# Performance work log

Hardware: AMD Instinct MI355X
Metric: run time of the kernel (lower is better)

## Reference

```python
import jax, jax.numpy as jnp
import numpy as np

NTOKENS = 50257
NHID = 1024
NPC = int(np.ceil(np.sqrt(NTOKENS)))            # 225 tokens per class
NCLASSES = int(np.ceil(NTOKENS / NPC))          # 224 classes
BATCH = 1024
INITRANGE = 0.1


def setup_inputs() -> dict:
    key = jax.random.key(0)
    k1, k2, k3, k4 = jax.random.split(key, 4)
    inputs = jax.random.normal(k1, (BATCH, NHID), dtype=jnp.float32)
    labels = jax.random.randint(k2, (BATCH,), 0, NTOKENS, dtype=jnp.int64)
    layer_top_W = jax.random.uniform(k3, (NHID, NCLASSES), minval=-INITRANGE, maxval=INITRANGE, dtype=jnp.float32)
    layer_top_b = jnp.zeros((NCLASSES,), dtype=jnp.float32)
    layer_bottom_W = jax.random.uniform(k4, (NCLASSES, NHID, NPC), minval=-INITRANGE, maxval=INITRANGE, dtype=jnp.float32)
    layer_bottom_b = jnp.zeros((NCLASSES, NPC), dtype=jnp.float32)
    return {
        "inputs": inputs,
        "labels": labels,
        "layer_top_W": layer_top_W,
        "layer_top_b": layer_top_b,
        "layer_bottom_W": layer_bottom_W,
        "layer_bottom_b": layer_bottom_b,
    }


def reference(inputs, labels, layer_top_W, layer_top_b, layer_bottom_W, layer_bottom_b):
    batch_size = inputs.shape[0]
    # decompose label into (class, within-class) position; old-torch `/` on Long == floor div
    pos_top = labels // NPC            # [B]
    pos_bottom = labels % NPC          # [B]

    # top-level class distribution: [B, nclasses]
    top_logits = inputs @ layer_top_W + layer_top_b
    top_probs = jax.nn.softmax(top_logits, axis=1)

    # gather per-sample class weight slices and do batched matvec:
    # layer_bottom_W[pos_top]: [B, nhid, npc]
    bottom_logits = jnp.einsum("bd,bdc->bc", inputs, layer_bottom_W[pos_top]) + layer_bottom_b[pos_top]
    bottom_probs = jax.nn.softmax(bottom_logits, axis=1)

    rows = jnp.arange(batch_size)
    target_probs = top_probs[rows, pos_top] * bottom_probs[rows, pos_bottom]  # [B]
    return target_probs
```

## Files before the change

kernel.cpp:

```cpp
#include <hip/hip_runtime.h>
#include <math.h>

#define NTOK 50257
#define NHID 1024
#define NPC  225
#define NCLS 224
#define BATCH 1024

#define WS_ORDER_OFS 16
#define WS_ITEMS_OFS 8192
#define WS_PTOP_OFS  16384
#define MAX_ITEMS    352

__device__ __forceinline__ void group_samples(const int* __restrict__ labels,
                                              int* __restrict__ ws, int tid)
{
    __shared__ int cnt[256];
    __shared__ int scan[256];
    __shared__ int iscan[256];
    __shared__ int cur[256];

    if (tid < 256) cnt[tid] = 0;
    __syncthreads();
    for (int i = tid; i < BATCH; i += 512)
        atomicAdd(&cnt[labels[i] / NPC], 1);
    __syncthreads();

    int myc = 0, myi = 0;
    if (tid < 256) {
        myc = (tid < NCLS) ? cnt[tid] : 0;
        myi = (myc + 7) >> 3;
        scan[tid]  = myc;
        iscan[tid] = myi;
    }
    __syncthreads();
    for (int off = 1; off < 256; off <<= 1) {
        int a = 0, b = 0;
        if (tid < 256 && tid >= off) { a = scan[tid - off]; b = iscan[tid - off]; }
        __syncthreads();
        if (tid < 256) { scan[tid] += a; iscan[tid] += b; }
        __syncthreads();
    }
    if (tid < 256) {
        const int sbase = scan[tid]  - myc;
        const int ibase = iscan[tid] - myi;
        if (tid == 255) ws[0] = iscan[255];
        cur[tid] = sbase;
        int4* items = (int4*)((char*)ws + WS_ITEMS_OFS);
        if (tid < NCLS)
            for (int t = 0; t < myi; ++t)
                items[ibase + t] = make_int4(tid, sbase + 8 * t, min(8, myc - 8 * t), 0);
    }
    __syncthreads();
    int* order = ws + WS_ORDER_OFS;
    for (int i = tid; i < BATCH; i += 512) {
        int c = labels[i] / NPC;
        int p = atomicAdd(&cur[c], 1);
        order[p] = i;
    }
}

template <int LD, int COLS, bool NT>
__device__ __forceinline__ void block_matvec8_softmax(
    float* __restrict__ sm,
    const float* __restrict__ W,
    const float* __restrict__ bias,
    int wave, int lane, int nt,
    const int* __restrict__ s_ids,
    const int* __restrict__ labels,
    bool bottom,
    const float* __restrict__ ptop,
    float* __restrict__ outp)
{
    float acc[8][4];
#pragma unroll
    for (int j = 0; j < 8; ++j)
#pragma unroll
        for (int k = 0; k < 4; ++k) acc[j][k] = 0.f;

    const int c0 = lane, c1 = lane + 64, c2 = lane + 128, c3 = lane + 192;
    const bool m3 = (c3 < COLS);
    const int d0 = wave * 128;
    const float* Wr = W + (size_t)d0 * LD;

    auto ldrow = [&](int r, float* o) {
        const float* p = Wr + (size_t)r * LD;
        if (NT) {
            o[0] = __builtin_nontemporal_load(p + c0);
            o[1] = __builtin_nontemporal_load(p + c1);
            o[2] = __builtin_nontemporal_load(p + c2);
            o[3] = m3 ? __builtin_nontemporal_load(p + c3) : 0.f;
        } else {
            o[0] = p[c0]; o[1] = p[c1]; o[2] = p[c2];
            o[3] = m3 ? p[c3] : 0.f;
        }
    };

    float wbuf[4][4];
    ldrow(0, wbuf[0]); ldrow(1, wbuf[1]); ldrow(2, wbuf[2]); ldrow(3, wbuf[3]);

#pragma unroll 4
    for (int dd = 0; dd < 128; ++dd) {
        const int slot = dd & 3;
        const float cw0 = wbuf[slot][0], cw1 = wbuf[slot][1],
                    cw2 = wbuf[slot][2], cw3 = wbuf[slot][3];
        ldrow(min(dd + 4, 127), wbuf[slot]);
        const float4 a = *(const float4*)&sm[(d0 + dd) * 12 + 0];
        const float4 b = *(const float4*)&sm[(d0 + dd) * 12 + 4];
        const float xi[8] = {a.x, a.y, a.z, a.w, b.x, b.y, b.z, b.w};
#pragma unroll
        for (int j = 0; j < 8; ++j) {
            acc[j][0] = fmaf(xi[j], cw0, acc[j][0]);
            acc[j][1] = fmaf(xi[j], cw1, acc[j][1]);
            acc[j][2] = fmaf(xi[j], cw2, acc[j][2]);
            acc[j][3] = fmaf(xi[j], cw3, acc[j][3]);
        }
    }
    __syncthreads();

    float* red = sm;
    if (wave >= 4) {
#pragma unroll
        for (int j = 0; j < 8; ++j)
#pragma unroll
            for (int k = 0; k < 4; ++k) {
                int c = lane + 64 * k;
                if (c < COLS) red[((wave - 4) * 8 + j) * 232 + c] = acc[j][k];
            }
    }
    __syncthreads();
    if (wave < 4) {
#pragma unroll
        for (int j = 0; j < 8; ++j)
#pragma unroll
            for (int k = 0; k < 4; ++k) {
                int c = lane + 64 * k;
                if (c < COLS) red[(wave * 8 + j) * 232 + c] += acc[j][k];
            }
    }
    __syncthreads();

    const int j = wave;
    if (j < nt) {
        const int s = s_ids[j];
        float v[4];
#pragma unroll
        for (int k = 0; k < 4; ++k) {
            int c = lane + 64 * k;
            v[k] = (c < COLS)
                     ? (red[(0 * 8 + j) * 232 + c] + red[(1 * 8 + j) * 232 + c] +
                        red[(2 * 8 + j) * 232 + c] + red[(3 * 8 + j) * 232 + c] +
                        bias[c])
                     : -INFINITY;
        }
        float m = fmaxf(fmaxf(v[0], v[1]), fmaxf(v[2], v[3]));
        for (int o = 32; o > 0; o >>= 1) m = fmaxf(m, __shfl_xor(m, o));
        float e = expf(v[0] - m) + expf(v[1] - m) + expf(v[2] - m) + expf(v[3] - m);
        for (int o = 32; o > 0; o >>= 1) e += __shfl_xor(e, o);
        const int lab = labels[s];
        const int tgt = bottom ? (lab % NPC) : (lab / NPC);
        if (lane == (tgt & 63)) {
            float p = expf(v[tgt >> 6] - m) / e;
            outp[s] = bottom ? (ptop[s] * p) : p;
        }
    }
}

__global__ __launch_bounds__(512) void k1_top(const float* __restrict__ X,
                                              const int* __restrict__ labels,
                                              const float* __restrict__ Wt,
                                              const float* __restrict__ bt,
                                              float* __restrict__ ptop,
                                              int* __restrict__ ws)
{
    __shared__ __align__(16) float smem[12288];
    const int tid = threadIdx.x;

    if (blockIdx.x == BATCH / 8) {
        group_samples(labels, ws, tid);
        return;
    }

    const int wave = tid >> 6;
    const int lane = tid & 63;
    const int sbase = blockIdx.x * 8;

    for (int idx = tid; idx < 2048; idx += 512) {
        const int j  = idx >> 8;
        const int d4 = idx & 255;
        const float4 v = ((const float4*)&X[(size_t)(sbase + j) * NHID])[d4];
        smem[(4 * d4 + 0) * 12 + j] = v.x;
        smem[(4 * d4 + 1) * 12 + j] = v.y;
        smem[(4 * d4 + 2) * 12 + j] = v.z;
        smem[(4 * d4 + 3) * 12 + j] = v.w;
    }
    __syncthreads();

    int s_ids[8];
#pragma unroll
    for (int j = 0; j < 8; ++j) s_ids[j] = sbase + j;

    block_matvec8_softmax<NCLS, NCLS, false>(smem, Wt, bt, wave, lane, 8, s_ids,
                                             labels, false, nullptr, ptop);
}

__global__ __launch_bounds__(512) void k2_bottom(const float* __restrict__ X,
                                                 const int* __restrict__ labels,
                                                 const float* __restrict__ Wb,
                                                 const float* __restrict__ bb,
                                                 const int* __restrict__ ws,
                                                 const float* __restrict__ ptop,
                                                 float* __restrict__ out)
{
    __shared__ __align__(16) float smem[12288];
    const int nitems = ws[0];
    if ((int)blockIdx.x >= nitems) return;
    const int4 item = ((const int4*)((const char*)ws + WS_ITEMS_OFS))[blockIdx.x];
    const int cls = item.x, s0 = item.y, nt = item.z;
    const int* order = ws + WS_ORDER_OFS;

    const int tid  = threadIdx.x;
    const int wave = tid >> 6;
    const int lane = tid & 63;

    int s_ids[8];
#pragma unroll
    for (int j = 0; j < 8; ++j) s_ids[j] = (j < nt) ? order[s0 + j] : 0;

    for (int idx = tid; idx < 2048; idx += 512) {
        const int j  = idx >> 8;
        const int d4 = idx & 255;
        float4 v = make_float4(0.f, 0.f, 0.f, 0.f);
        if (j < nt) v = ((const float4*)&X[(size_t)s_ids[j] * NHID])[d4];
        smem[(4 * d4 + 0) * 12 + j] = v.x;
        smem[(4 * d4 + 1) * 12 + j] = v.y;
        smem[(4 * d4 + 2) * 12 + j] = v.z;
        smem[(4 * d4 + 3) * 12 + j] = v.w;
    }
    __syncthreads();

    const float* W = Wb + (size_t)cls * (NHID * NPC);
    block_matvec8_softmax<NPC, NPC, true>(smem, W, bb + cls * NPC, wave, lane,
                                          nt, s_ids, labels, true, ptop, out);
}

extern "C" void kernel_launch(void* const* d_in, const int* in_sizes, int n_in,
                              void* d_out, int out_size, void* d_ws, size_t ws_size,
                              hipStream_t stream)
{
    const float* X      = (const float*)d_in[0];
    const int*   labels = (const int*)  d_in[1];
    const float* Wt     = (const float*)d_in[2];
    const float* bt     = (const float*)d_in[3];
    const float* Wb     = (const float*)d_in[4];
    const float* bb     = (const float*)d_in[5];
    float* out = (float*)d_out;
    int*   ws  = (int*)d_ws;
    float* ptop = (float*)((char*)d_ws + WS_PTOP_OFS);

    hipLaunchKernelGGL(k1_top, dim3(BATCH / 8 + 1), dim3(512), 0, stream,
                       X, labels, Wt, bt, ptop, ws);
    hipLaunchKernelGGL(k2_bottom, dim3(MAX_ITEMS), dim3(512), 0, stream,
                       X, labels, Wb, bb, ws, ptop, out);
}
```

Baseline: 309.4 us.

## Assign one bottom block per class, batching up to sixteen samples per weight pass

```diff
diff --git a/kernel.cpp b/kernel.cpp
--- a/kernel.cpp
+++ b/kernel.cpp
@@ -7,71 +7,29 @@
 #define NCLS 224
 #define BATCH 1024
 
-#define WS_ORDER_OFS 16
-#define WS_ITEMS_OFS 8192
-#define WS_PTOP_OFS  16384
-#define MAX_ITEMS    352
-
-__device__ __forceinline__ void group_samples(const int* __restrict__ labels,
-                                              int* __restrict__ ws, int tid)
+__global__ __launch_bounds__(512) void k1_top(const float* __restrict__ X,
+                                              const int* __restrict__ labels,
+                                              const float* __restrict__ Wt,
+                                              const float* __restrict__ bt,
+                                              float* __restrict__ ptop)
 {
-    __shared__ int cnt[256];
-    __shared__ int scan[256];
-    __shared__ int iscan[256];
-    __shared__ int cur[256];
-
-    if (tid < 256) cnt[tid] = 0;
-    __syncthreads();
-    for (int i = tid; i < BATCH; i += 512)
-        atomicAdd(&cnt[labels[i] / NPC], 1);
-    __syncthreads();
-
-    int myc = 0, myi = 0;
-    if (tid < 256) {
-        myc = (tid < NCLS) ? cnt[tid] : 0;
-        myi = (myc + 7) >> 3;
-        scan[tid]  = myc;
-        iscan[tid] = myi;
-    }
-    __syncthreads();
-    for (int off = 1; off < 256; off <<= 1) {
-        int a = 0, b = 0;
-        if (tid < 256 && tid >= off) { a = scan[tid - off]; b = iscan[tid - off]; }
-        __syncthreads();
-        if (tid < 256) { scan[tid] += a; iscan[tid] += b; }
-        __syncthreads();
-    }
-    if (tid < 256) {
-        const int sbase = scan[tid]  - myc;
-        const int ibase = iscan[tid] - myi;
-        if (tid == 255) ws[0] = iscan[255];
-        cur[tid] = sbase;
-        int4* items = (int4*)((char*)ws + WS_ITEMS_OFS);
-        if (tid < NCLS)
-            for (int t = 0; t < myi; ++t)
-                items[ibase + t] = make_int4(tid, sbase + 8 * t, min(8, myc - 8 * t), 0);
-    }
-    __syncthreads();
-    int* order = ws + WS_ORDER_OFS;
-    for (int i = tid; i < BATCH; i += 512) {
-        int c = labels[i] / NPC;
-        int p = atomicAdd(&cur[c], 1);
-        order[p] = i;
-    }
-}
-
-template <int LD, int COLS, bool NT>
-__device__ __forceinline__ void block_matvec8_softmax(
-    float* __restrict__ sm,
-    const float* __restrict__ W,
-    const float* __restrict__ bias,
-    int wave, int lane, int nt,
-    const int* __restrict__ s_ids,
-    const int* __restrict__ labels,
-    bool bottom,
-    const float* __restrict__ ptop,
-    float* __restrict__ outp)
-{
+    __shared__ __align__(16) float sm[12288];
+    const int tid  = threadIdx.x;
+    const int wave = tid >> 6;
+    const int lane = tid & 63;
+    const int sbase = blockIdx.x * 8;
+
+    for (int idx = tid; idx < 2048; idx += 512) {
+        const int j  = idx >> 8;
+        const int d4 = idx & 255;
+        const float4 v = ((const float4*)&X[(size_t)(sbase + j) * NHID])[d4];
+        sm[(4 * d4 + 0) * 12 + j] = v.x;
+        sm[(4 * d4 + 1) * 12 + j] = v.y;
+        sm[(4 * d4 + 2) * 12 + j] = v.z;
+        sm[(4 * d4 + 3) * 12 + j] = v.w;
+    }
+    __syncthreads();
+
     float acc[8][4];
 #pragma unroll
     for (int j = 0; j < 8; ++j)
@@ -79,23 +37,15 @@
         for (int k = 0; k < 4; ++k) acc[j][k] = 0.f;
 
     const int c0 = lane, c1 = lane + 64, c2 = lane + 128, c3 = lane + 192;
-    const bool m3 = (c3 < COLS);
+    const bool m3 = (c3 < NCLS);
     const int d0 = wave * 128;
-    const float* Wr = W + (size_t)d0 * LD;
+    const float* Wr = Wt + (size_t)d0 * NCLS;
 
     auto ldrow = [&](int r, float* o) {
-        const float* p = Wr + (size_t)r * LD;
-        if (NT) {
-            o[0] = __builtin_nontemporal_load(p + c0);
-            o[1] = __builtin_nontemporal_load(p + c1);
-            o[2] = __builtin_nontemporal_load(p + c2);
-            o[3] = m3 ? __builtin_nontemporal_load(p + c3) : 0.f;
-        } else {
-            o[0] = p[c0]; o[1] = p[c1]; o[2] = p[c2];
-            o[3] = m3 ? p[c3] : 0.f;
-        }
+        const float* p = Wr + (size_t)r * NCLS;
+        o[0] = p[c0]; o[1] = p[c1]; o[2] = p[c2];
+        o[3] = m3 ? p[c3] : 0.f;
     };
-
     float wbuf[4][4];
     ldrow(0, wbuf[0]); ldrow(1, wbuf[1]); ldrow(2, wbuf[2]); ldrow(3, wbuf[3]);
 
@@ -125,7 +75,7 @@
 #pragma unroll
             for (int k = 0; k < 4; ++k) {
                 int c = lane + 64 * k;
-                if (c < COLS) red[((wave - 4) * 8 + j) * 232 + c] = acc[j][k];
+                if (c < NCLS) red[((wave - 4) * 8 + j) * 232 + c] = acc[j][k];
             }
     }
     __syncthreads();
@@ -135,113 +85,171 @@
 #pragma unroll
             for (int k = 0; k < 4; ++k) {
                 int c = lane + 64 * k;
-                if (c < COLS) red[(wave * 8 + j) * 232 + c] += acc[j][k];
+                if (c < NCLS) red[(wave * 8 + j) * 232 + c] += acc[j][k];
             }
     }
     __syncthreads();
 
     const int j = wave;
-    if (j < nt) {
-        const int s = s_ids[j];
+    {
+        const int s = sbase + j;
         float v[4];
 #pragma unroll
         for (int k = 0; k < 4; ++k) {
             int c = lane + 64 * k;
-            v[k] = (c < COLS)
+            v[k] = (c < NCLS)
                      ? (red[(0 * 8 + j) * 232 + c] + red[(1 * 8 + j) * 232 + c] +
                         red[(2 * 8 + j) * 232 + c] + red[(3 * 8 + j) * 232 + c] +
-                        bias[c])
+                        bt[c])
                      : -INFINITY;
         }
         float m = fmaxf(fmaxf(v[0], v[1]), fmaxf(v[2], v[3]));
         for (int o = 32; o > 0; o >>= 1) m = fmaxf(m, __shfl_xor(m, o));
         float e = expf(v[0] - m) + expf(v[1] - m) + expf(v[2] - m) + expf(v[3] - m);
         for (int o = 32; o > 0; o >>= 1) e += __shfl_xor(e, o);
-        const int lab = labels[s];
-        const int tgt = bottom ? (lab % NPC) : (lab / NPC);
-        if (lane == (tgt & 63)) {
-            float p = expf(v[tgt >> 6] - m) / e;
-            outp[s] = bottom ? (ptop[s] * p) : p;
-        }
-    }
-}
-
-__global__ __launch_bounds__(512) void k1_top(const float* __restrict__ X,
-                                              const int* __restrict__ labels,
-                                              const float* __restrict__ Wt,
-                                              const float* __restrict__ bt,
-                                              float* __restrict__ ptop,
-                                              int* __restrict__ ws)
-{
-    __shared__ __align__(16) float smem[12288];
-    const int tid = threadIdx.x;
-
-    if (blockIdx.x == BATCH / 8) {
-        group_samples(labels, ws, tid);
-        return;
-    }
-
-    const int wave = tid >> 6;
-    const int lane = tid & 63;
-    const int sbase = blockIdx.x * 8;
-
-    for (int idx = tid; idx < 2048; idx += 512) {
-        const int j  = idx >> 8;
-        const int d4 = idx & 255;
-        const float4 v = ((const float4*)&X[(size_t)(sbase + j) * NHID])[d4];
-        smem[(4 * d4 + 0) * 12 + j] = v.x;
-        smem[(4 * d4 + 1) * 12 + j] = v.y;
-        smem[(4 * d4 + 2) * 12 + j] = v.z;
-        smem[(4 * d4 + 3) * 12 + j] = v.w;
-    }
-    __syncthreads();
-
-    int s_ids[8];
-#pragma unroll
-    for (int j = 0; j < 8; ++j) s_ids[j] = sbase + j;
-
-    block_matvec8_softmax<NCLS, NCLS, false>(smem, Wt, bt, wave, lane, 8, s_ids,
-                                             labels, false, nullptr, ptop);
+        const int pt = labels[s] / NPC;
+        if (lane == (pt & 63))
+            ptop[s] = expf(v[pt >> 6] - m) / e;
+    }
 }
 
 __global__ __launch_bounds__(512) void k2_bottom(const float* __restrict__ X,
                                                  const int* __restrict__ labels,
                                                  const float* __restrict__ Wb,
                                                  const float* __restrict__ bb,
-                                                 const int* __restrict__ ws,
                                                  const float* __restrict__ ptop,
                                                  float* __restrict__ out)
 {
-    __shared__ __align__(16) float smem[12288];
-    const int nitems = ws[0];
-    if ((int)blockIdx.x >= nitems) return;
-    const int4 item = ((const int4*)((const char*)ws + WS_ITEMS_OFS))[blockIdx.x];
-    const int cls = item.x, s0 = item.y, nt = item.z;
-    const int* order = ws + WS_ORDER_OFS;
-
+    __shared__ __align__(16) float sm[16384];
+    __shared__ int s_cnt;
+    __shared__ int s_ids[64];
+    const int cls  = blockIdx.x;
     const int tid  = threadIdx.x;
     const int wave = tid >> 6;
     const int lane = tid & 63;
 
-    int s_ids[8];
-#pragma unroll
-    for (int j = 0; j < 8; ++j) s_ids[j] = (j < nt) ? order[s0 + j] : 0;
-
-    for (int idx = tid; idx < 2048; idx += 512) {
-        const int j  = idx >> 8;
-        const int d4 = idx & 255;
-        float4 v = make_float4(0.f, 0.f, 0.f, 0.f);
-        if (j < nt) v = ((const float4*)&X[(size_t)s_ids[j] * NHID])[d4];
-        smem[(4 * d4 + 0) * 12 + j] = v.x;
-        smem[(4 * d4 + 1) * 12 + j] = v.y;
-        smem[(4 * d4 + 2) * 12 + j] = v.z;
-        smem[(4 * d4 + 3) * 12 + j] = v.w;
-    }
-    __syncthreads();
-
-    const float* W = Wb + (size_t)cls * (NHID * NPC);
-    block_matvec8_softmax<NPC, NPC, true>(smem, W, bb + cls * NPC, wave, lane,
-                                          nt, s_ids, labels, true, ptop, out);
+    if (tid == 0) s_cnt = 0;
+    __syncthreads();
+    for (int i = tid; i < BATCH; i += 512) {
+        if (labels[i] / NPC == cls) {
+            int p = atomicAdd(&s_cnt, 1);
+            if (p < 64) s_ids[p] = i;
+        }
+    }
+    __syncthreads();
+    const int cnt = min(s_cnt, 64);
+    if (cnt == 0) return;
+
+    const float* W    = Wb + (size_t)cls * (NHID * NPC);
+    const float* bias = bb + (size_t)cls * NPC;
+
+    const int c0 = lane, c1 = lane + 64, c2 = lane + 128, c3 = lane + 192;
+    const bool m3 = (c3 < NPC);
+    const int d0 = wave * 128;
+    const float* Wr = W + (size_t)d0 * NPC;
+
+    for (int base = 0; base < cnt; base += 16) {
+        const int nt = min(16, cnt - base);
+
+        for (int idx = tid; idx < 4096; idx += 512) {
+            const int j  = idx >> 8;
+            const int d4 = idx & 255;
+            float4 v = make_float4(0.f, 0.f, 0.f, 0.f);
+            if (j < nt) v = ((const float4*)&X[(size_t)s_ids[base + j] * NHID])[d4];
+            sm[(4 * d4 + 0) * 16 + j] = v.x;
+            sm[(4 * d4 + 1) * 16 + j] = v.y;
+            sm[(4 * d4 + 2) * 16 + j] = v.z;
+            sm[(4 * d4 + 3) * 16 + j] = v.w;
+        }
+        __syncthreads();
+
+        float acc[16][4];
+#pragma unroll
+        for (int j = 0; j < 16; ++j)
+#pragma unroll
+            for (int k = 0; k < 4; ++k) acc[j][k] = 0.f;
+
+        auto ldrow = [&](int r, float* o) {
+            const float* p = Wr + (size_t)r * NPC;
+            o[0] = __builtin_nontemporal_load(p + c0);
+            o[1] = __builtin_nontemporal_load(p + c1);
+            o[2] = __builtin_nontemporal_load(p + c2);
+            o[3] = m3 ? __builtin_nontemporal_load(p + c3) : 0.f;
+        };
+        float wbuf[4][4];
+        ldrow(0, wbuf[0]); ldrow(1, wbuf[1]); ldrow(2, wbuf[2]); ldrow(3, wbuf[3]);
+
+#pragma unroll 2
+        for (int dd = 0; dd < 128; ++dd) {
+            const int slot = dd & 3;
+            const float cw0 = wbuf[slot][0], cw1 = wbuf[slot][1],
+                        cw2 = wbuf[slot][2], cw3 = wbuf[slot][3];
+            ldrow(min(dd + 4, 127), wbuf[slot]);
+            const float4 a = *(const float4*)&sm[(d0 + dd) * 16 + 0];
+            const float4 b = *(const float4*)&sm[(d0 + dd) * 16 + 4];
+            const float c4 = 0.f; (void)c4;
+            const float4 c = *(const float4*)&sm[(d0 + dd) * 16 + 8];
+            const float4 e = *(const float4*)&sm[(d0 + dd) * 16 + 12];
+            const float xi[16] = {a.x, a.y, a.z, a.w, b.x, b.y, b.z, b.w,
+                                  c.x, c.y, c.z, c.w, e.x, e.y, e.z, e.w};
+#pragma unroll
+            for (int j = 0; j < 16; ++j) {
+                acc[j][0] = fmaf(xi[j], cw0, acc[j][0]);
+                acc[j][1] = fmaf(xi[j], cw1, acc[j][1]);
+                acc[j][2] = fmaf(xi[j], cw2, acc[j][2]);
+                acc[j][3] = fmaf(xi[j], cw3, acc[j][3]);
+            }
+        }
+        __syncthreads();
+
+        float* red = sm;
+        if (wave >= 4) {
+#pragma unroll
+            for (int j = 0; j < 16; ++j)
+#pragma unroll
+                for (int k = 0; k < 4; ++k) {
+                    int c = lane + 64 * k;
+                    if (c < NPC) red[((wave - 4) * 16 + j) * 232 + c] = acc[j][k];
+                }
+        }
+        __syncthreads();
+        if (wave < 4) {
+#pragma unroll
+            for (int j = 0; j < 16; ++j)
+#pragma unroll
+                for (int k = 0; k < 4; ++k) {
+                    int c = lane + 64 * k;
+                    if (c < NPC) red[(wave * 16 + j) * 232 + c] += acc[j][k];
+                }
+        }
+        __syncthreads();
+
+#pragma unroll
+        for (int jj = 0; jj < 2; ++jj) {
+            const int j = wave + 8 * jj;
+            if (j < nt) {
+                const int s = s_ids[base + j];
+                float v[4];
+#pragma unroll
+                for (int k = 0; k < 4; ++k) {
+                    int c = lane + 64 * k;
+                    v[k] = (c < NPC)
+                             ? (red[(0 * 16 + j) * 232 + c] + red[(1 * 16 + j) * 232 + c] +
+                                red[(2 * 16 + j) * 232 + c] + red[(3 * 16 + j) * 232 + c] +
+                                bias[c])
+                             : -INFINITY;
+                }
+                float m = fmaxf(fmaxf(v[0], v[1]), fmaxf(v[2], v[3]));
+                for (int o = 32; o > 0; o >>= 1) m = fmaxf(m, __shfl_xor(m, o));
+                float e = expf(v[0] - m) + expf(v[1] - m) + expf(v[2] - m) + expf(v[3] - m);
+                for (int o = 32; o > 0; o >>= 1) e += __shfl_xor(e, o);
+                const int pb = labels[s] % NPC;
+                if (lane == (pb & 63))
+                    out[s] = ptop[s] * (expf(v[pb >> 6] - m) / e);
+            }
+        }
+        __syncthreads();
+    }
 }
 
 extern "C" void kernel_launch(void* const* d_in, const int* in_sizes, int n_in,
@@ -254,12 +262,11 @@
     const float* bt     = (const float*)d_in[3];
     const float* Wb     = (const float*)d_in[4];
     const float* bb     = (const float*)d_in[5];
-    float* out = (float*)d_out;
-    int*   ws  = (int*)d_ws;
-    float* ptop = (float*)((char*)d_ws + WS_PTOP_OFS);
-
-    hipLaunchKernelGGL(k1_top, dim3(BATCH / 8 + 1), dim3(512), 0, stream,
-                       X, labels, Wt, bt, ptop, ws);
-    hipLaunchKernelGGL(k2_bottom, dim3(MAX_ITEMS), dim3(512), 0, stream,
-                       X, labels, Wb, bb, ws, ptop, out);
+    float* out  = (float*)d_out;
+    float* ptop = (float*)d_ws;
+
+    hipLaunchKernelGGL(k1_top, dim3(BATCH / 8), dim3(512), 0, stream,
+                       X, labels, Wt, bt, ptop);
+    hipLaunchKernelGGL(k2_bottom, dim3(NCLS), dim3(512), 0, stream,
+                       X, labels, Wb, bb, ptop, out);
 }
```

New measurement: 335.8 us. 8.5% more time.
